# Optimization experiments

Measured on AMD Instinct MI355X. Metric: run time of the kernel, lower is better.

## Reference

```python
import jax, jax.numpy as jnp
import numpy as np

D1, D2, B, I, O = 64, 64, 32, 64, 128


def setup_inputs() -> dict:
    key = jax.random.key(0)
    ks = jax.random.split(key, 13)
    k = float(np.sqrt(1.0 / O))
    u = lambda kk, shape: jax.random.uniform(kk, shape, minval=-k, maxval=k, dtype=jnp.float32)
    return {
        "x": jax.random.normal(ks[0], (D1, D2, B, I), dtype=jnp.float32),
        "wf": u(ks[1], (2, I, O)),
        "uf": u(ks[2], (2, 2, O)),
        "biasf": u(ks[3], (2, O)),
        "wi": u(ks[4], (I, O)),
        "ui": u(ks[5], (2, O)),
        "biasi": u(ks[6], (O,)),
        "wo": u(ks[7], (I, O)),
        "uo": u(ks[8], (2, O)),
        "biaso": u(ks[9], (O,)),
        "wc": u(ks[10], (I, O)),
        "uc": u(ks[11], (2, O)),
        "biasc": u(ks[12], (O,)),
    }


def reference(x, wf, uf, biasf, wi, ui, biasi, wo, uo, biaso, wc, uc, biasc):
    # x: (D1, D2, B, I). Recurrence: cell (i,j) depends on (i-1,j) [k=0] and (i,j-1) [k=1].
    d1, d2, b, _ = x.shape
    o_dim = wi.shape[1]

    def cell(xj, s0, h0):
        # s0, h0: (2, B, O); index 0 = up-neighbor (dim 0), 1 = left-neighbor (dim 1)
        f = jax.nn.sigmoid(biasf[:, None, :]
                           + jnp.einsum('bi,lio->lbo', xj, wf)
                           + jnp.einsum('kbo,lko->lbo', h0, uf))
        i = jax.nn.sigmoid(biasi + xj @ wi + (h0 * ui[:, None, :]).sum(0))
        og = jax.nn.sigmoid(biaso + xj @ wo + (h0 * uo[:, None, :]).sum(0))
        c = jax.nn.sigmoid(biasc + xj @ wc + (h0 * uc[:, None, :]).sum(0))  # note: sigmoid, as in source
        s = i * c + (f * s0).sum(0)
        h = og * jnp.tanh(s)
        return s, h

    z_row = jnp.zeros((d2, b, o_dim), x.dtype)
    z = jnp.zeros((b, o_dim), x.dtype)

    def row_step(carry, x_row):
        s_up_row, h_up_row = carry  # (D2, B, O) each: previous row's states

        def col_step(c2, inp):
            s_left, h_left = c2
            xj, s_up, h_up = inp
            s, h = cell(xj, jnp.stack([s_up, s_left]), jnp.stack([h_up, h_left]))
            return (s, h), (s, h)

        _, (s_row, h_row) = jax.lax.scan(col_step, (z, z), (x_row, s_up_row, h_up_row))
        return (s_row, h_row), s_row

    _, s_all = jax.lax.scan(row_step, (z_row, z_row), x)
    # Original module returns reshape(s, ...) (cell state), not h -- reproduce faithfully.
    return s_all  # (D1, D2, B, O)
```

## Files before the change

kernel.cpp:

```cpp
#include <hip/hip_runtime.h>
#include <hip/hip_fp16.h>


#define GX_ELEMS ((size_t)32 * 5 * 128 * 4096)

typedef __attribute__((ext_vector_type(8))) _Float16 half8;
typedef __attribute__((ext_vector_type(4))) float f32x4;

__device__ __forceinline__ int diag_off(int d) {
    return (d < 64) ? ((d * (d + 1)) >> 1) : (4096 - (((127 - d) * (128 - d)) >> 1));
}

__global__ __launch_bounds__(256) void lut_kernel(int* __restrict__ lut) {
    int t = blockIdx.x * 256 + threadIdx.x;
    int i = t >> 6, j = t & 63;
    int d = i + j;
    int jmin = (d > 63) ? (d - 63) : 0;
    lut[diag_off(d) + j - jmin] = t;
}

__global__ __launch_bounds__(256) void prep_w(
    const float* __restrict__ wf, const float* __restrict__ wi,
    const float* __restrict__ wo, const float* __restrict__ wc,
    _Float16* __restrict__ wt)
{
    const int g = blockIdx.x;
    const float* W = (g == 0) ? wf : (g == 1) ? (wf + 8192)
                   : (g == 2) ? wi : (g == 3) ? wo : wc;
    const int t = threadIdx.x;
    const int o = t >> 1, k0 = (t & 1) * 32;
    _Float16 buf[32];
#pragma unroll
    for (int k = 0; k < 32; ++k) buf[k] = (_Float16)(-W[(k0 + k) * 128 + o]);
    _Float16* dst = wt + ((size_t)g * 128 + o) * 64 + k0;
#pragma unroll
    for (int q = 0; q < 4; ++q) *(half8*)(dst + q * 8) = *(half8*)(buf + q * 8);
}

__global__ __launch_bounds__(256) void gemm_kernel(
    const float* __restrict__ x, const _Float16* __restrict__ wt,
    const float* __restrict__ biasf, const float* __restrict__ biasi,
    const float* __restrict__ biaso, const float* __restrict__ biasc,
    const int* __restrict__ lut, __half* __restrict__ gx)
{
    __shared__ _Float16 As[128][72];
    __shared__ _Float16 BC[128 * 136];

    const int t  = threadIdx.x;
    const int p0 = blockIdx.x * 128;
    const int b  = blockIdx.y;

    {
        int r = t >> 1, k0 = (t & 1) * 32;
        int cell = lut[p0 + r];
        const float* xr = x + ((size_t)cell * 32 + b) * 64 + k0;
#pragma unroll
        for (int it = 0; it < 4; ++it) {
            float4 v0 = *(const float4*)(xr + it * 8);
            float4 v1 = *(const float4*)(xr + it * 8 + 4);
            half8 h;
            h[0] = (_Float16)v0.x; h[1] = (_Float16)v0.y;
            h[2] = (_Float16)v0.z; h[3] = (_Float16)v0.w;
            h[4] = (_Float16)v1.x; h[5] = (_Float16)v1.y;
            h[6] = (_Float16)v1.z; h[7] = (_Float16)v1.w;
            *(half8*)&As[r][k0 + it * 8] = h;
        }
    }

    const int lane = t & 63;
    const int wv   = __builtin_amdgcn_readfirstlane(t >> 6);
    const int m    = lane & 15;
    const int quad = lane >> 4;

    for (int g = 0; g < 5; ++g) {
        const float* bias = (g == 0) ? biasf : (g == 1) ? (biasf + 128)
                          : (g == 2) ? biasi : (g == 3) ? biaso : biasc;
        __syncthreads();
        {
            const _Float16* wg = wt + (size_t)g * 8192;
#pragma unroll
            for (int q = 0; q < 4; ++q) {
                int f = t * 4 + q;
                int o = f >> 3, c = (f & 7) * 8;
                *(half8*)&BC[o * 72 + c] = *(const half8*)(wg + o * 64 + c);
            }
        }
        __syncthreads();
        half8 bf0[2], bf1[2];
#pragma unroll
        for (int kh = 0; kh < 2; ++kh) {
            bf0[kh] = *(half8*)&BC[(wv * 32 + m) * 72 + kh * 32 + quad * 8];
            bf1[kh] = *(half8*)&BC[(wv * 32 + 16 + m) * 72 + kh * 32 + quad * 8];
        }
        __syncthreads();
        f32x4 acc[8][2] = {};
#pragma unroll
        for (int kh = 0; kh < 2; ++kh) {
#pragma unroll
            for (int pf = 0; pf < 8; ++pf) {
                half8 af = *(half8*)&As[pf * 16 + m][kh * 32 + quad * 8];
                acc[pf][0] = __builtin_amdgcn_mfma_f32_16x16x32_f16(af, bf0[kh], acc[pf][0], 0, 0, 0);
                acc[pf][1] = __builtin_amdgcn_mfma_f32_16x16x32_f16(af, bf1[kh], acc[pf][1], 0, 0, 0);
            }
        }
        float sb0 = -bias[wv * 32 + m];
        float sb1 = -bias[wv * 32 + 16 + m];
#pragma unroll
        for (int pf = 0; pf < 8; ++pf) {
#pragma unroll
            for (int of = 0; of < 2; ++of) {
                int o  = wv * 32 + of * 16 + m;
                int pc = pf * 16 + quad * 4;
                float sb = of ? sb1 : sb0;
                __half2 lo = __floats2half2_rn(acc[pf][of][0] + sb, acc[pf][of][1] + sb);
                __half2 hi = __floats2half2_rn(acc[pf][of][2] + sb, acc[pf][of][3] + sb);
                uint2 pk;
                pk.x = *(unsigned*)&lo;
                pk.y = *(unsigned*)&hi;
                *(uint2*)&BC[o * 136 + pc] = pk;
            }
        }
        __syncthreads();
        __half* gbase = gx + ((size_t)(b * 5 + g) * 128) * 4096 + p0;
#pragma unroll
        for (int it = 0; it < 8; ++it) {
            int o = it * 16 + (t >> 4);
            int c = (t & 15) * 8;
            *(half8*)(gbase + (size_t)o * 4096 + c) = *(half8*)&BC[o * 136 + c];
        }
    }
}

__global__ __launch_bounds__(256) void recur_kernel(
    __half* gx,
    const float* __restrict__ uf, const float* __restrict__ ui,
    const float* __restrict__ uo, const float* __restrict__ uc)
{
    const int lane = threadIdx.x & 63;
    const int w = __builtin_amdgcn_readfirstlane(blockIdx.x * 4 + (threadIdx.x >> 6));
    const int b = w >> 7, o = w & 127;

    const float nf00 = -uf[o],       nf01 = -uf[128 + o];
    const float nf10 = -uf[256 + o], nf11 = -uf[384 + o];
    const float ni0 = -ui[o], ni1 = -ui[128 + o];
    const float no0 = -uo[o], no1 = -uo[128 + o];
    const float nc0 = -uc[o], nc1 = -uc[128 + o];

    char* base = (char*)(gx + ((size_t)(b * 5) * 128 + o) * 4096);
    const int SL  = 128 * 4096 * 2;
    const int l2  = lane * 2;
    const int zm  = (lane == 0) ? 0 : -1;
    const int bpi = (lane - 1) * 4;

    int svb = 0;
    int sob = 0;
    float c0,c1,c2,c3,c4, n0,n1,n2,n3,n4;

#define LD5(v0_,v1_,v2_,v3_,v4_)                                   \
    { const char* p_ = base + svb;                                 \
      v0_ = (float)*(const _Float16*)(p_ + l2);                    \
      v1_ = (float)*(const _Float16*)(p_ + SL + l2);               \
      v2_ = (float)*(const _Float16*)(p_ + 2 * SL + l2);           \
      v3_ = (float)*(const _Float16*)(p_ + 3 * SL + l2);           \
      v4_ = (float)*(const _Float16*)(p_ + 4 * SL + l2); }

    LD5(c0,c1,c2,c3,c4); svb += 2;
    LD5(n0,n1,n2,n3,n4); svb += 4;

    float s_prev = 0.f, h_prev = 0.f;

    for (int d = 0; d < 127; ++d) {
        float t0,t1,t2,t3,t4;
        LD5(t0,t1,t2,t3,t4);
        int del = min(d + 3, 124 - d); del = max(del, 0);
        svb += del * 2;

        int slb = __builtin_amdgcn_ds_bpermute(bpi, __float_as_int(s_prev)) & zm;
        int hlb = __builtin_amdgcn_ds_bpermute(bpi, __float_as_int(h_prev)) & zm;
        float sl = __int_as_float(slb), hl = __int_as_float(hlb);

        float zf0 = fmaf(h_prev, nf00, fmaf(hl, nf01, c0));
        float zf1 = fmaf(h_prev, nf10, fmaf(hl, nf11, c1));
        float zi  = fmaf(h_prev, ni0,  fmaf(hl, ni1,  c2));
        float zo  = fmaf(h_prev, no0,  fmaf(hl, no1,  c3));
        float zc  = fmaf(h_prev, nc0,  fmaf(hl, nc1,  c4));
        float f0 = __builtin_amdgcn_rcpf(1.f + __expf(zf0));
        float f1 = __builtin_amdgcn_rcpf(1.f + __expf(zf1));
        float ig = __builtin_amdgcn_rcpf(1.f + __expf(zi));
        float og = __builtin_amdgcn_rcpf(1.f + __expf(zo));
        float cg = __builtin_amdgcn_rcpf(1.f + __expf(zc));

        float s  = fmaf(ig, cg, fmaf(f0, s_prev, f1 * sl));
        float e2 = __expf(s + s);
        float th = fmaf(-2.f, __builtin_amdgcn_rcpf(1.f + e2), 1.f);
        float h  = og * th;

        bool act = (unsigned)(d - lane) < 64u;
        if (act) *(_Float16*)(base + sob + l2) = (_Float16)s;
        sob += min(d + 1, 126 - d) * 2;

        s_prev = act ? s : 0.f;
        h_prev = act ? h : 0.f;
        c0 = n0; c1 = n1; c2 = n2; c3 = n3; c4 = n4;
        n0 = t0; n1 = t1; n2 = t2; n3 = t3; n4 = t4;
    }
#undef LD5
}

__global__ __launch_bounds__(256) void transpose_kernel(
    const __half* __restrict__ gx, const int* __restrict__ lut,
    float* __restrict__ out)
{
    __shared__ _Float16 T[256][80];
    const int t  = threadIdx.x;
    const int p0 = blockIdx.x * 64;
    const int w0 = blockIdx.y * 256;
#pragma unroll
    for (int it = 0; it < 8; ++it) {
        int wl = it * 32 + (t >> 3), pl = (t & 7) * 8;
        int w = w0 + wl;
        int row = (w >> 7) * 640 + (w & 127);
        *(half8*)&T[wl][pl] =
            *(const half8*)((const _Float16*)gx + (size_t)row * 4096 + p0 + pl);
    }
    __syncthreads();
    float* ob = out + w0 + t;
#pragma unroll 4
    for (int p = 0; p < 64; ++p) {
        int cell = lut[p0 + p];
        ob[(size_t)cell * 4096] = (float)T[t][p];
    }
}

extern "C" void kernel_launch(void* const* d_in, const int* in_sizes, int n_in,
                              void* d_out, int out_size, void* d_ws, size_t ws_size,
                              hipStream_t stream) {
    const float* x     = (const float*)d_in[0];
    const float* wf    = (const float*)d_in[1];
    const float* uf    = (const float*)d_in[2];
    const float* biasf = (const float*)d_in[3];
    const float* wi    = (const float*)d_in[4];
    const float* ui    = (const float*)d_in[5];
    const float* biasi = (const float*)d_in[6];
    const float* wo    = (const float*)d_in[7];
    const float* uo    = (const float*)d_in[8];
    const float* biaso = (const float*)d_in[9];
    const float* wc    = (const float*)d_in[10];
    const float* uc    = (const float*)d_in[11];
    const float* biasc = (const float*)d_in[12];
    float* out = (float*)d_out;

    __half*   gx  = (__half*)d_ws;
    int*      lut = (int*)((char*)d_ws + GX_ELEMS * sizeof(__half));
    _Float16* wt  = (_Float16*)((char*)lut + 16384);

    lut_kernel<<<16, 256, 0, stream>>>(lut);
    prep_w<<<5, 256, 0, stream>>>(wf, wi, wo, wc, wt);
    gemm_kernel<<<dim3(32, 32), 256, 0, stream>>>(
        x, wt, biasf, biasi, biaso, biasc, lut, gx);
    recur_kernel<<<1024, 256, 0, stream>>>(gx, uf, ui, uo, uc);
    transpose_kernel<<<dim3(64, 16), 256, 0, stream>>>(gx, lut, out);
}
```

Before: 248.0 us.

## Interleave gate pre-activations in pairs and fold log2e into weights

The GEMM now writes gate planes f0/f1 and i/o as interleaved half pairs, plus a separate c plane. The recurrence kernel therefore issues three loads per diagonal step instead of five. The GEMM stages weights directly from global into registers, dropping the LDS staging and the transposed write-back through shared memory. It stores output rows directly, which may be less coalesced. Weights, biases and recurrent coefficients are prescaled by log2(e) so the sigmoid and tanh use native exp2. Rounding changes to round-toward-zero packing.

```diff
diff --git a/kernel.cpp b/kernel.cpp
--- a/kernel.cpp
+++ b/kernel.cpp
@@ -2,10 +2,20 @@
 #include <hip/hip_fp16.h>
 
 
-#define GX_ELEMS ((size_t)32 * 5 * 128 * 4096)
+#define P23_OFF  ((size_t)64 << 20)
+#define P4_OFF   ((size_t)128 << 20)
+#define GX_BYTES ((size_t)160 << 20)
+#define LOG2E    1.4426950408889634f
 
 typedef __attribute__((ext_vector_type(8))) _Float16 half8;
+typedef __attribute__((ext_vector_type(2))) __fp16 fp16x2;
 typedef __attribute__((ext_vector_type(4))) float f32x4;
+
+__device__ __forceinline__ unsigned pkrtz(float a, float b) {
+    union { fp16x2 h; unsigned u; } c;
+    c.h = __builtin_amdgcn_cvt_pkrtz(a, b);
+    return c.u;
+}
 
 __device__ __forceinline__ int diag_off(int d) {
     return (d < 64) ? ((d * (d + 1)) >> 1) : (4096 - (((127 - d) * (128 - d)) >> 1));
@@ -31,21 +41,20 @@
     const int o = t >> 1, k0 = (t & 1) * 32;
     _Float16 buf[32];
 #pragma unroll
-    for (int k = 0; k < 32; ++k) buf[k] = (_Float16)(-W[(k0 + k) * 128 + o]);
+    for (int k = 0; k < 32; ++k)
+        buf[k] = (_Float16)(-W[(k0 + k) * 128 + o] * LOG2E);
     _Float16* dst = wt + ((size_t)g * 128 + o) * 64 + k0;
 #pragma unroll
     for (int q = 0; q < 4; ++q) *(half8*)(dst + q * 8) = *(half8*)(buf + q * 8);
 }
 
-__global__ __launch_bounds__(256) void gemm_kernel(
+__global__ __launch_bounds__(256, 2) void gemm_kernel(
     const float* __restrict__ x, const _Float16* __restrict__ wt,
     const float* __restrict__ biasf, const float* __restrict__ biasi,
     const float* __restrict__ biaso, const float* __restrict__ biasc,
-    const int* __restrict__ lut, __half* __restrict__ gx)
+    const int* __restrict__ lut, char* __restrict__ gx)
 {
     __shared__ _Float16 As[128][72];
-    __shared__ _Float16 BC[128 * 136];
-
     const int t  = threadIdx.x;
     const int p0 = blockIdx.x * 128;
     const int b  = blockIdx.y;
@@ -66,114 +75,143 @@
             *(half8*)&As[r][k0 + it * 8] = h;
         }
     }
+    __syncthreads();
 
     const int lane = t & 63;
     const int wv   = __builtin_amdgcn_readfirstlane(t >> 6);
     const int m    = lane & 15;
     const int quad = lane >> 4;
-
-    for (int g = 0; g < 5; ++g) {
-        const float* bias = (g == 0) ? biasf : (g == 1) ? (biasf + 128)
-                          : (g == 2) ? biasi : (g == 3) ? biaso : biasc;
-        __syncthreads();
-        {
-            const _Float16* wg = wt + (size_t)g * 8192;
-#pragma unroll
-            for (int q = 0; q < 4; ++q) {
-                int f = t * 4 + q;
-                int o = f >> 3, c = (f & 7) * 8;
-                *(half8*)&BC[o * 72 + c] = *(const half8*)(wg + o * 64 + c);
+    const int o0   = wv * 32 + m;
+    const int o1   = o0 + 16;
+    const size_t row0 = (size_t)(b * 128 + o0) * 4096;
+    const size_t row1 = (size_t)(b * 128 + o1) * 4096;
+    const int pq = p0 + quad * 4;
+
+    auto pair_phase = [&](const _Float16* wga, const _Float16* wgb,
+                          const float* bA, const float* bB, char* plane) {
+        half8 ba0[2], ba1[2], bb0[2], bb1[2];
+#pragma unroll
+        for (int kh = 0; kh < 2; ++kh) {
+            ba0[kh] = *(const half8*)(wga + o0 * 64 + kh * 32 + quad * 8);
+            ba1[kh] = *(const half8*)(wga + o1 * 64 + kh * 32 + quad * 8);
+            bb0[kh] = *(const half8*)(wgb + o0 * 64 + kh * 32 + quad * 8);
+            bb1[kh] = *(const half8*)(wgb + o1 * 64 + kh * 32 + quad * 8);
+        }
+        f32x4 aA[8][2] = {}, aB[8][2] = {};
+#pragma unroll
+        for (int pf = 0; pf < 8; ++pf) {
+            half8 af0 = *(const half8*)&As[pf * 16 + m][quad * 8];
+            half8 af1 = *(const half8*)&As[pf * 16 + m][32 + quad * 8];
+            aA[pf][0] = __builtin_amdgcn_mfma_f32_16x16x32_f16(af0, ba0[0], aA[pf][0], 0, 0, 0);
+            aA[pf][0] = __builtin_amdgcn_mfma_f32_16x16x32_f16(af1, ba0[1], aA[pf][0], 0, 0, 0);
+            aA[pf][1] = __builtin_amdgcn_mfma_f32_16x16x32_f16(af0, ba1[0], aA[pf][1], 0, 0, 0);
+            aA[pf][1] = __builtin_amdgcn_mfma_f32_16x16x32_f16(af1, ba1[1], aA[pf][1], 0, 0, 0);
+            aB[pf][0] = __builtin_amdgcn_mfma_f32_16x16x32_f16(af0, bb0[0], aB[pf][0], 0, 0, 0);
+            aB[pf][0] = __builtin_amdgcn_mfma_f32_16x16x32_f16(af1, bb0[1], aB[pf][0], 0, 0, 0);
+            aB[pf][1] = __builtin_amdgcn_mfma_f32_16x16x32_f16(af0, bb1[0], aB[pf][1], 0, 0, 0);
+            aB[pf][1] = __builtin_amdgcn_mfma_f32_16x16x32_f16(af1, bb1[1], aB[pf][1], 0, 0, 0);
+        }
+        float sA0 = -bA[o0] * LOG2E, sA1 = -bA[o1] * LOG2E;
+        float sB0 = -bB[o0] * LOG2E, sB1 = -bB[o1] * LOG2E;
+#pragma unroll
+        for (int pf = 0; pf < 8; ++pf) {
+#pragma unroll
+            for (int of = 0; of < 2; ++of) {
+                float sa = of ? sA1 : sA0, sb = of ? sB1 : sB0;
+                f32x4 va = aA[pf][of], vb = aB[pf][of];
+                uint4 st;
+                st.x = pkrtz(va[0] + sa, vb[0] + sb);
+                st.y = pkrtz(va[1] + sa, vb[1] + sb);
+                st.z = pkrtz(va[2] + sa, vb[2] + sb);
+                st.w = pkrtz(va[3] + sa, vb[3] + sb);
+                size_t row = of ? row1 : row0;
+                *(uint4*)(plane + (row + pq + pf * 16) * 4) = st;
             }
         }
-        __syncthreads();
-        half8 bf0[2], bf1[2];
+    };
+    pair_phase(wt,            wt + 8192,     biasf, biasf + 128, gx);
+    pair_phase(wt + 2 * 8192, wt + 3 * 8192, biasi, biaso,       gx + P23_OFF);
+
+    {
+        const _Float16* wg = wt + 4 * 8192;
+        half8 b0[2], b1[2];
 #pragma unroll
         for (int kh = 0; kh < 2; ++kh) {
-            bf0[kh] = *(half8*)&BC[(wv * 32 + m) * 72 + kh * 32 + quad * 8];
-            bf1[kh] = *(half8*)&BC[(wv * 32 + 16 + m) * 72 + kh * 32 + quad * 8];
-        }
-        __syncthreads();
-        f32x4 acc[8][2] = {};
-#pragma unroll
-        for (int kh = 0; kh < 2; ++kh) {
-#pragma unroll
-            for (int pf = 0; pf < 8; ++pf) {
-                half8 af = *(half8*)&As[pf * 16 + m][kh * 32 + quad * 8];
-                acc[pf][0] = __builtin_amdgcn_mfma_f32_16x16x32_f16(af, bf0[kh], acc[pf][0], 0, 0, 0);
-                acc[pf][1] = __builtin_amdgcn_mfma_f32_16x16x32_f16(af, bf1[kh], acc[pf][1], 0, 0, 0);
+            b0[kh] = *(const half8*)(wg + o0 * 64 + kh * 32 + quad * 8);
+            b1[kh] = *(const half8*)(wg + o1 * 64 + kh * 32 + quad * 8);
+        }
+        f32x4 ac[8][2] = {};
+#pragma unroll
+        for (int pf = 0; pf < 8; ++pf) {
+            half8 af0 = *(const half8*)&As[pf * 16 + m][quad * 8];
+            half8 af1 = *(const half8*)&As[pf * 16 + m][32 + quad * 8];
+            ac[pf][0] = __builtin_amdgcn_mfma_f32_16x16x32_f16(af0, b0[0], ac[pf][0], 0, 0, 0);
+            ac[pf][0] = __builtin_amdgcn_mfma_f32_16x16x32_f16(af1, b0[1], ac[pf][0], 0, 0, 0);
+            ac[pf][1] = __builtin_amdgcn_mfma_f32_16x16x32_f16(af0, b1[0], ac[pf][1], 0, 0, 0);
+            ac[pf][1] = __builtin_amdgcn_mfma_f32_16x16x32_f16(af1, b1[1], ac[pf][1], 0, 0, 0);
+        }
+        float s0 = -biasc[o0] * LOG2E, s1 = -biasc[o1] * LOG2E;
+        char* plane = gx + P4_OFF;
+#pragma unroll
+        for (int pf = 0; pf < 8; ++pf) {
+#pragma unroll
+            for (int of = 0; of < 2; ++of) {
+                float sb = of ? s1 : s0;
+                f32x4 v = ac[pf][of];
+                uint2 st;
+                st.x = pkrtz(v[0] + sb, v[1] + sb);
+                st.y = pkrtz(v[2] + sb, v[3] + sb);
+                size_t row = of ? row1 : row0;
+                *(uint2*)(plane + (row + pq + pf * 16) * 2) = st;
             }
         }
-        float sb0 = -bias[wv * 32 + m];
-        float sb1 = -bias[wv * 32 + 16 + m];
-#pragma unroll
-        for (int pf = 0; pf < 8; ++pf) {
-#pragma unroll
-            for (int of = 0; of < 2; ++of) {
-                int o  = wv * 32 + of * 16 + m;
-                int pc = pf * 16 + quad * 4;
-                float sb = of ? sb1 : sb0;
-                __half2 lo = __floats2half2_rn(acc[pf][of][0] + sb, acc[pf][of][1] + sb);
-                __half2 hi = __floats2half2_rn(acc[pf][of][2] + sb, acc[pf][of][3] + sb);
-                uint2 pk;
-                pk.x = *(unsigned*)&lo;
-                pk.y = *(unsigned*)&hi;
-                *(uint2*)&BC[o * 136 + pc] = pk;
-            }
-        }
-        __syncthreads();
-        __half* gbase = gx + ((size_t)(b * 5 + g) * 128) * 4096 + p0;
-#pragma unroll
-        for (int it = 0; it < 8; ++it) {
-            int o = it * 16 + (t >> 4);
-            int c = (t & 15) * 8;
-            *(half8*)(gbase + (size_t)o * 4096 + c) = *(half8*)&BC[o * 136 + c];
-        }
     }
 }
 
 __global__ __launch_bounds__(256) void recur_kernel(
-    __half* gx,
+    char* __restrict__ gx,
     const float* __restrict__ uf, const float* __restrict__ ui,
     const float* __restrict__ uo, const float* __restrict__ uc)
 {
     const int lane = threadIdx.x & 63;
     const int w = __builtin_amdgcn_readfirstlane(blockIdx.x * 4 + (threadIdx.x >> 6));
-    const int b = w >> 7, o = w & 127;
-
-    const float nf00 = -uf[o],       nf01 = -uf[128 + o];
-    const float nf10 = -uf[256 + o], nf11 = -uf[384 + o];
-    const float ni0 = -ui[o], ni1 = -ui[128 + o];
-    const float no0 = -uo[o], no1 = -uo[128 + o];
-    const float nc0 = -uc[o], nc1 = -uc[128 + o];
-
-    char* base = (char*)(gx + ((size_t)(b * 5) * 128 + o) * 4096);
-    const int SL  = 128 * 4096 * 2;
-    const int l2  = lane * 2;
+    const int o = w & 127;
+
+    const float nf00 = -uf[o] * LOG2E,       nf01 = -uf[128 + o] * LOG2E;
+    const float nf10 = -uf[256 + o] * LOG2E, nf11 = -uf[384 + o] * LOG2E;
+    const float ni0 = -ui[o] * LOG2E, ni1 = -ui[128 + o] * LOG2E;
+    const float no0 = -uo[o] * LOG2E, no1 = -uo[128 + o] * LOG2E;
+    const float nc0 = -uc[o] * LOG2E, nc1 = -uc[128 + o] * LOG2E;
+
+    const char* pc01 = gx + (size_t)w * 16384;
+    const char* pc23 = gx + P23_OFF + (size_t)w * 16384;
+    const char* pc4  = gx + P4_OFF + (size_t)w * 8192;
+    char*       ps4  = gx + P4_OFF + (size_t)w * 8192;
+    const int l4 = lane * 4, l2 = lane * 2;
+
     const int zm  = (lane == 0) ? 0 : -1;
     const int bpi = (lane - 1) * 4;
 
-    int svb = 0;
-    int sob = 0;
     float c0,c1,c2,c3,c4, n0,n1,n2,n3,n4;
 
-#define LD5(v0_,v1_,v2_,v3_,v4_)                                   \
-    { const char* p_ = base + svb;                                 \
-      v0_ = (float)*(const _Float16*)(p_ + l2);                    \
-      v1_ = (float)*(const _Float16*)(p_ + SL + l2);               \
-      v2_ = (float)*(const _Float16*)(p_ + 2 * SL + l2);           \
-      v3_ = (float)*(const _Float16*)(p_ + 3 * SL + l2);           \
-      v4_ = (float)*(const _Float16*)(p_ + 4 * SL + l2); }
-
-    LD5(c0,c1,c2,c3,c4); svb += 2;
-    LD5(n0,n1,n2,n3,n4); svb += 4;
+#define LD3(v0_,v1_,v2_,v3_,v4_) { \
+    __half2 h01 = *(const __half2*)(pc01 + l4); \
+    __half2 h23 = *(const __half2*)(pc23 + l4); \
+    _Float16 h4 = *(const _Float16*)(pc4 + l2); \
+    v0_ = __low2float(h01); v1_ = __high2float(h01); \
+    v2_ = __low2float(h23); v3_ = __high2float(h23); \
+    v4_ = (float)h4; }
+
+    LD3(c0,c1,c2,c3,c4); pc01 += 4;  pc23 += 4;  pc4 += 2;
+    LD3(n0,n1,n2,n3,n4); pc01 += 8;  pc23 += 8;  pc4 += 4;
 
     float s_prev = 0.f, h_prev = 0.f;
 
     for (int d = 0; d < 127; ++d) {
         float t0,t1,t2,t3,t4;
-        LD5(t0,t1,t2,t3,t4);
+        LD3(t0,t1,t2,t3,t4);
         int del = min(d + 3, 124 - d); del = max(del, 0);
-        svb += del * 2;
+        pc01 += del * 4; pc23 += del * 4; pc4 += del * 2;
 
         int slb = __builtin_amdgcn_ds_bpermute(bpi, __float_as_int(s_prev)) & zm;
         int hlb = __builtin_amdgcn_ds_bpermute(bpi, __float_as_int(h_prev)) & zm;
@@ -184,44 +222,43 @@
         float zi  = fmaf(h_prev, ni0,  fmaf(hl, ni1,  c2));
         float zo  = fmaf(h_prev, no0,  fmaf(hl, no1,  c3));
         float zc  = fmaf(h_prev, nc0,  fmaf(hl, nc1,  c4));
-        float f0 = __builtin_amdgcn_rcpf(1.f + __expf(zf0));
-        float f1 = __builtin_amdgcn_rcpf(1.f + __expf(zf1));
-        float ig = __builtin_amdgcn_rcpf(1.f + __expf(zi));
-        float og = __builtin_amdgcn_rcpf(1.f + __expf(zo));
-        float cg = __builtin_amdgcn_rcpf(1.f + __expf(zc));
+        float f0 = __builtin_amdgcn_rcpf(1.f + __builtin_amdgcn_exp2f(zf0));
+        float f1 = __builtin_amdgcn_rcpf(1.f + __builtin_amdgcn_exp2f(zf1));
+        float ig = __builtin_amdgcn_rcpf(1.f + __builtin_amdgcn_exp2f(zi));
+        float og = __builtin_amdgcn_rcpf(1.f + __builtin_amdgcn_exp2f(zo));
+        float cg = __builtin_amdgcn_rcpf(1.f + __builtin_amdgcn_exp2f(zc));
 
         float s  = fmaf(ig, cg, fmaf(f0, s_prev, f1 * sl));
-        float e2 = __expf(s + s);
+        float e2 = __builtin_amdgcn_exp2f(s * (2.f * LOG2E));
         float th = fmaf(-2.f, __builtin_amdgcn_rcpf(1.f + e2), 1.f);
         float h  = og * th;
 
         bool act = (unsigned)(d - lane) < 64u;
-        if (act) *(_Float16*)(base + sob + l2) = (_Float16)s;
-        sob += min(d + 1, 126 - d) * 2;
+        if (act) *(_Float16*)(ps4 + l2) = (_Float16)s;
+        ps4 += min(d + 1, 126 - d) * 2;
 
         s_prev = act ? s : 0.f;
         h_prev = act ? h : 0.f;
         c0 = n0; c1 = n1; c2 = n2; c3 = n3; c4 = n4;
         n0 = t0; n1 = t1; n2 = t2; n3 = t3; n4 = t4;
     }
-#undef LD5
+#undef LD3
 }
 
 __global__ __launch_bounds__(256) void transpose_kernel(
-    const __half* __restrict__ gx, const int* __restrict__ lut,
+    const char* __restrict__ gx, const int* __restrict__ lut,
     float* __restrict__ out)
 {
     __shared__ _Float16 T[256][80];
+    const _Float16* p4 = (const _Float16*)(gx + P4_OFF);
     const int t  = threadIdx.x;
     const int p0 = blockIdx.x * 64;
     const int w0 = blockIdx.y * 256;
 #pragma unroll
     for (int it = 0; it < 8; ++it) {
         int wl = it * 32 + (t >> 3), pl = (t & 7) * 8;
-        int w = w0 + wl;
-        int row = (w >> 7) * 640 + (w & 127);
         *(half8*)&T[wl][pl] =
-            *(const half8*)((const _Float16*)gx + (size_t)row * 4096 + p0 + pl);
+            *(const half8*)(p4 + (size_t)(w0 + wl) * 4096 + p0 + pl);
     }
     __syncthreads();
     float* ob = out + w0 + t;
@@ -250,8 +287,8 @@
     const float* biasc = (const float*)d_in[12];
     float* out = (float*)d_out;
 
-    __half*   gx  = (__half*)d_ws;
-    int*      lut = (int*)((char*)d_ws + GX_ELEMS * sizeof(__half));
+    char*     gx  = (char*)d_ws;
+    int*      lut = (int*)(gx + GX_BYTES);
     _Float16* wt  = (_Float16*)((char*)lut + 16384);
 
     lut_kernel<<<16, 256, 0, stream>>>(lut);
```

Result: faster. 240.5 us (-3.0%).
